# Kernel tuning notes

Measured on AMD Instinct MI355X. Metric: run time of the kernel, lower is better.

Reference implementation:

```python
import jax, jax.numpy as jnp
import numpy as np

B, T = 8, 2048
IN, OUT = 1024, 1024
M, C = 32, 32
MIN_P, MAX_P = 1.0, 1024.0
EPS = 1e-5


def setup_inputs() -> dict:
    key = jax.random.key(0)
    ks = jax.random.split(key, 4)
    x = jax.random.normal(ks[0], (B, T, IN), dtype=jnp.float32)
    # pre: Linear(IN, 2*M + 2*OUT); mix: Linear(2*M*C, OUT)
    pre_w = jax.random.normal(ks[1], (IN, 2 * M + 2 * OUT), dtype=jnp.float32) / np.sqrt(IN)
    pre_b = jnp.zeros((2 * M + 2 * OUT,), jnp.float32)
    mix_w = jax.random.normal(ks[2], (2 * M * C, OUT), dtype=jnp.float32) / np.sqrt(2 * M * C)
    mix_b = jnp.zeros((OUT,), jnp.float32)
    # FFA decay/oscillation params (paper init): gamma_{m,c} = exp(-|a_m| + i b_c)
    a = jnp.linspace(1e-6, 0.5, M, dtype=jnp.float32)
    b = 2.0 * jnp.pi / jnp.linspace(MIN_P, MAX_P, C, dtype=jnp.float32)
    return dict(x=x, pre_w=pre_w, pre_b=pre_b, mix_w=mix_w, mix_b=mix_b, a=a, b=b)


def _ffa(u, a, b):
    """Complex-decay linear recurrence: s_t = gamma * s_{t-1} + u_t (s_0 = 0).

    u: [B,T,M] real input (broadcast over context dim C).
    Returns all states: [B,T,M,C] complex64.
    """
    log_gamma = (-jnp.abs(a))[:, None] + 1j * b[None, :]  # [M,C]
    gamma = jnp.exp(log_gamma).astype(jnp.complex64)
    Tn = u.shape[1]
    h = jnp.broadcast_to(u[..., None].astype(jnp.complex64), u.shape + (C,))  # [B,T,M,C]
    h = jnp.moveaxis(h, 1, 0)  # [T,B,M,C]
    p = jnp.broadcast_to(gamma, (Tn, 1, M, C))  # [T,1,M,C] time-invariant decay

    def combine(e1, e2):
        p1, h1 = e1
        p2, h2 = e2
        return (p1 * p2, h1 * p2 + h2)

    _, hs = jax.lax.associative_scan(combine, (p, h), axis=0)
    return jnp.moveaxis(hs, 0, 1)  # [B,T,M,C]


def reference(x, pre_w, pre_b, mix_w, mix_b, a, b):
    Bx, Tx, _ = x.shape
    pre = x @ pre_w + pre_b  # [B,T,2M+2OUT]
    y, thru, gate = jnp.split(pre, [M, M + OUT], axis=-1)
    gate = jax.nn.sigmoid(gate)
    in_gate, out_gate = gate[..., :M], gate[..., M:]
    s = _ffa(y * in_gate, a, b)  # [B,T,M,C] complex64
    # torch.view_as_real -> [...,M,C,2] then flatten -> interleaved (re,im)
    zr = jnp.stack([s.real, s.imag], axis=-1).reshape(Bx, Tx, 2 * M * C)
    z = zr @ mix_w + mix_b  # [B,T,OUT]
    # LayerNorm (no affine)
    z = (z - z.mean(-1, keepdims=True)) / jnp.sqrt(z.var(-1, keepdims=True) + EPS)
    out = z * out_gate + thru * (1.0 - out_gate)
    return out, s
```

## Files before the change

### kernel.cpp

```cpp
#include <hip/hip_runtime.h>
#include <stdint.h>

typedef __attribute__((ext_vector_type(2))) __bf16 bf16x2;
typedef __attribute__((ext_vector_type(4))) __bf16 bf16x4;
typedef __attribute__((ext_vector_type(8))) __bf16 bf16x8;
typedef __attribute__((ext_vector_type(4))) float f32x4;

#define DEV __device__ __forceinline__

DEV void g2lds16(const void* g, void* l) {
  __builtin_amdgcn_global_load_lds(
      (const __attribute__((address_space(1))) void*)g,
      (__attribute__((address_space(3))) void*)l, 16, 0, 0);
}

__global__ __launch_bounds__(256) void cvt_f32_bf16(const float* __restrict__ s,
                                                    __bf16* __restrict__ d, int n) {
  int i = (blockIdx.x * 256 + threadIdx.x) * 4;
  if (i >= n) return;
  float4 v = *reinterpret_cast<const float4*>(s + i);
  bf16x4 o;
  o[0] = (__bf16)v.x; o[1] = (__bf16)v.y; o[2] = (__bf16)v.z; o[3] = (__bf16)v.w;
  *reinterpret_cast<bf16x4*>(d + i) = o;
}

__global__ __launch_bounds__(256) void transpose_to_bf16(const float* __restrict__ src,
                                                         __bf16* __restrict__ dst,
                                                         int K, int N, int Npad) {
  __shared__ float tile[32][33];
  int n0 = blockIdx.x * 32, k0 = blockIdx.y * 32;
  int tx = threadIdx.x & 31, ty = threadIdx.x >> 5;
#pragma unroll
  for (int j = 0; j < 4; ++j) {
    int k = k0 + ty + j * 8;
    int n = n0 + tx;
    float v = 0.f;
    if (n < N) v = src[(long)k * N + n];
    tile[ty + j * 8][tx] = v;
  }
  __syncthreads();
#pragma unroll
  for (int j = 0; j < 4; ++j) {
    int n = n0 + ty + j * 8;
    int k = k0 + tx;
    if (n < Npad) dst[(long)n * K + k] = (__bf16)tile[tx][ty + j * 8];
  }
}

template <bool OUT_BF16>
__global__ __launch_bounds__(256) void gemm_mfma(const __bf16* __restrict__ A,
                                                 const __bf16* __restrict__ Wt,
                                                 const float* __restrict__ bias,
                                                 void* __restrict__ Cout,
                                                 int K, int Nreal, int ldc) {
  __shared__ __bf16 As[2][128 * 32];
  __shared__ __bf16 Bs[2][128 * 32];
  const int tid = threadIdx.x;
  const int lane = tid & 63, wid = tid >> 6;

  const int nwg = gridDim.x * gridDim.y;
  const int orig = blockIdx.y * gridDim.x + blockIdx.x;
  const int wg = ((orig & 7) * (nwg >> 3)) + (orig >> 3);
  const int tm = (wg / gridDim.x) * 128, tn = (wg % gridDim.x) * 128;

  const int wr = (wid >> 1) * 64, wc = (wid & 1) * 64;

  f32x4 acc[4][4] = {};

  const int r0 = tid >> 2, c0 = (tid & 3) * 8;
  const int r1 = r0 + 64;

  int aoff[4], boff[4];
#pragma unroll
  for (int i = 0; i < 4; ++i) {
    aoff[i] = (wr + i * 16 + (lane & 15)) * 32 + (lane >> 4) * 8;
    boff[i] = (wc + i * 16 + (lane & 15)) * 32 + (lane >> 4) * 8;
  }

  const __bf16* Arow0 = A + (long)(tm + r0) * K + c0;
  const __bf16* Arow1 = A + (long)(tm + r1) * K + c0;
  const __bf16* Wrow0 = Wt + (long)(tn + r0) * K + c0;
  const __bf16* Wrow1 = Wt + (long)(tn + r1) * K + c0;

  g2lds16(Arow0, As[0] + tid * 8);
  g2lds16(Arow1, As[0] + (tid + 256) * 8);
  g2lds16(Wrow0, Bs[0] + tid * 8);
  g2lds16(Wrow1, Bs[0] + (tid + 256) * 8);
  __syncthreads();

  const int nt = K >> 5;
  int cur = 0;
  for (int t = 1; t < nt; ++t) {
    const int k0 = t << 5;
    const int nxt = cur ^ 1;
    g2lds16(Arow0 + k0, As[nxt] + tid * 8);
    g2lds16(Arow1 + k0, As[nxt] + (tid + 256) * 8);
    g2lds16(Wrow0 + k0, Bs[nxt] + tid * 8);
    g2lds16(Wrow1 + k0, Bs[nxt] + (tid + 256) * 8);
    bf16x8 af[4], bw[4];
#pragma unroll
    for (int i = 0; i < 4; ++i) af[i] = *reinterpret_cast<const bf16x8*>(&As[cur][aoff[i]]);
#pragma unroll
    for (int i = 0; i < 4; ++i) bw[i] = *reinterpret_cast<const bf16x8*>(&Bs[cur][boff[i]]);
#pragma unroll
    for (int mi = 0; mi < 4; ++mi)
#pragma unroll
      for (int ni = 0; ni < 4; ++ni)
        acc[mi][ni] = __builtin_amdgcn_mfma_f32_16x16x32_bf16(af[mi], bw[ni],
                                                              acc[mi][ni], 0, 0, 0);
    __syncthreads();
    cur = nxt;
  }
  {
    bf16x8 af[4], bw[4];
#pragma unroll
    for (int i = 0; i < 4; ++i) af[i] = *reinterpret_cast<const bf16x8*>(&As[cur][aoff[i]]);
#pragma unroll
    for (int i = 0; i < 4; ++i) bw[i] = *reinterpret_cast<const bf16x8*>(&Bs[cur][boff[i]]);
#pragma unroll
    for (int mi = 0; mi < 4; ++mi)
#pragma unroll
      for (int ni = 0; ni < 4; ++ni)
        acc[mi][ni] = __builtin_amdgcn_mfma_f32_16x16x32_bf16(af[mi], bw[ni],
                                                              acc[mi][ni], 0, 0, 0);
  }

  const int rbase = tm + wr + ((lane >> 4) * 4);
  const int cbase = tn + wc + (lane & 15);
#pragma unroll
  for (int mi = 0; mi < 4; ++mi) {
#pragma unroll
    for (int ni = 0; ni < 4; ++ni) {
      int col = cbase + ni * 16;
      if (col < Nreal) {
        float bv = bias[col];
#pragma unroll
        for (int r = 0; r < 4; ++r) {
          long row = rbase + mi * 16 + r;
          float v = acc[mi][ni][r] + bv;
          if (OUT_BF16) ((__bf16*)Cout)[row * ldc + col] = (__bf16)v;
          else          ((float*)Cout)[row * ldc + col] = v;
        }
      }
    }
  }
}

__global__ __launch_bounds__(256) void u_kernel(const __bf16* __restrict__ pre,
                                                float* __restrict__ u) {
  int i = blockIdx.x * 8 + (threadIdx.x >> 5);
  int m = threadIdx.x & 31;
  const __bf16* pr = pre + (long)i * 2112;
  float y = (float)pr[m];
  float g = (float)pr[1056 + m];
  float sg = 1.f / (1.f + expf(-g));
  int b = i >> 11, t = i & 2047;
  u[(long)((b * 32) + m) * 2048 + t] = y * sg;
}

__global__ __launch_bounds__(64) void scan_kernel(const float* __restrict__ u,
                                                  const float* __restrict__ a,
                                                  const float* __restrict__ bfr,
                                                  __bf16* __restrict__ s_bf,
                                                  float* __restrict__ s_re) {
  int blk = blockIdx.x;
  int b = blk >> 4, mp = blk & 15;
  int lane = threadIdx.x;
  int mh = lane >> 5, c = lane & 31;
  int m = mp * 2 + mh;
  const float* ub = u + (long)(b * 32 + m) * 2048;
  float decay = expf(-fabsf(a[m]));
  float gr = decay * cosf(bfr[c]);
  float gi = decay * sinf(bfr[c]);
  float sr = 0.f, si = 0.f;
  long base = (long)b * 2048 * 1024 + m * 32 + c;
  for (int t = 0; t < 2048; ++t) {
    float uv = ub[t];
    float nr = fmaf(gr, sr, fmaf(-gi, si, uv));
    float ni_ = fmaf(gr, si, gi * sr);
    sr = nr; si = ni_;
    long ci = base + (long)t * 1024;
    bf16x2 zv; zv[0] = (__bf16)sr; zv[1] = (__bf16)si;
    *reinterpret_cast<bf16x2*>(s_bf + 2 * ci) = zv;
    s_re[ci] = sr;
  }
}

__global__ __launch_bounds__(256) void ln_gate_kernel(float* __restrict__ z,
                                                      const __bf16* __restrict__ pre) {
  __shared__ float rs[4], rss[4];
  long row = blockIdx.x;
  float* zp = z + row * 1024;
  int tid = threadIdx.x;
  float4 v = *reinterpret_cast<const float4*>(zp + tid * 4);
  float s = v.x + v.y + v.z + v.w;
  float ss = v.x * v.x + v.y * v.y + v.z * v.z + v.w * v.w;
#pragma unroll
  for (int o = 32; o > 0; o >>= 1) {
    s += __shfl_down(s, o, 64);
    ss += __shfl_down(ss, o, 64);
  }
  if ((tid & 63) == 0) { rs[tid >> 6] = s; rss[tid >> 6] = ss; }
  __syncthreads();
  s = rs[0] + rs[1] + rs[2] + rs[3];
  ss = rss[0] + rss[1] + rss[2] + rss[3];
  float mean = s * (1.f / 1024.f);
  float var = ss * (1.f / 1024.f) - mean * mean;
  float rstd = rsqrtf(var + 1e-5f);
  const __bf16* pr = pre + row * 2112;
  bf16x4 th = *reinterpret_cast<const bf16x4*>(pr + 32 + tid * 4);
  bf16x4 og = *reinterpret_cast<const bf16x4*>(pr + 1088 + tid * 4);
  float4 o; float g;
  g = 1.f / (1.f + expf(-(float)og[0])); o.x = (v.x - mean) * rstd * g + (float)th[0] * (1.f - g);
  g = 1.f / (1.f + expf(-(float)og[1])); o.y = (v.y - mean) * rstd * g + (float)th[1] * (1.f - g);
  g = 1.f / (1.f + expf(-(float)og[2])); o.z = (v.z - mean) * rstd * g + (float)th[2] * (1.f - g);
  g = 1.f / (1.f + expf(-(float)og[3])); o.w = (v.w - mean) * rstd * g + (float)th[3] * (1.f - g);
  *reinterpret_cast<float4*>(zp + tid * 4) = o;
}

extern "C" void kernel_launch(void* const* d_in, const int* in_sizes, int n_in,
                              void* d_out, int out_size, void* d_ws, size_t ws_size,
                              hipStream_t stream) {
  const float* x = (const float*)d_in[0];
  const float* pre_w = (const float*)d_in[1];
  const float* pre_b = (const float*)d_in[2];
  const float* mix_w = (const float*)d_in[3];
  const float* mix_b = (const float*)d_in[4];
  const float* a = (const float*)d_in[5];
  const float* bfr = (const float*)d_in[6];

  char* ws = (char*)d_ws;
  __bf16* buf0  = (__bf16*)(ws + 0);
  __bf16* preWT = (__bf16*)(ws + 67108864);
  __bf16* mixWT = (__bf16*)(ws + 71565312);
  __bf16* pre   = (__bf16*)(ws + 75759616);
  float*  u     = (float*)(ws + 144965632);
  const size_t WS_NEEDED = 147062784ull;
  if (ws_size < WS_NEEDED) return;

  __bf16* x_bf = buf0;
  __bf16* s_bf = buf0;

  float* out0 = (float*)d_out;
  float* s_re = out0 + 16777216;

  cvt_f32_bf16<<<16384, 256, 0, stream>>>(x, x_bf, 16777216);
  transpose_to_bf16<<<dim3(68, 32), 256, 0, stream>>>(pre_w, preWT, 1024, 2112, 2176);
  transpose_to_bf16<<<dim3(32, 64), 256, 0, stream>>>(mix_w, mixWT, 2048, 1024, 1024);
  gemm_mfma<true><<<dim3(17, 128), 256, 0, stream>>>(x_bf, preWT, pre_b, pre,
                                                     1024, 2112, 2112);
  u_kernel<<<2048, 256, 0, stream>>>(pre, u);
  scan_kernel<<<128, 64, 0, stream>>>(u, a, bfr, s_bf, s_re);
  gemm_mfma<false><<<dim3(8, 128), 256, 0, stream>>>(s_bf, mixWT, mix_b, out0,
                                                     2048, 1024, 1024);
  ln_gate_kernel<<<16384, 256, 0, stream>>>(out0, pre);
}
```

Before: 361.3 us.

## Replace GEMM with 256x256-tile 8-wave kernel using phased LDS pipelining

Replaces the 128x128-tile, 4-wave bf16 MFMA GEMM with a 256x256-tile, 512-thread kernel. Each block stages 64-wide K chunks into double-buffered LDS with a swizzled layout, and splits the compute into four phases whose loads are interleaved with MFMAs using explicit barriers, waitcnts and setprio. The aim is more data reuse per LDS byte, fewer bank conflicts, and overlap of global-to-LDS copies with compute. The two weight transposes now share one workspace buffer, with the mix_w transpose moved after the first GEMM. Costs are higher register and LDS pressure and padding of the pre GEMM's N dimension to 2304, which wastes some work.

```diff
diff --git a/kernel.cpp b/kernel.cpp
--- a/kernel.cpp
+++ b/kernel.cpp
@@ -12,6 +12,14 @@
   __builtin_amdgcn_global_load_lds(
       (const __attribute__((address_space(1))) void*)g,
       (__attribute__((address_space(3))) void*)l, 16, 0, 0);
+}
+
+DEV void barrier_ws() {
+  __builtin_amdgcn_sched_barrier(0);
+  asm volatile("" ::: "memory");
+  __builtin_amdgcn_s_barrier();
+  asm volatile("" ::: "memory");
+  __builtin_amdgcn_sched_barrier(0);
 }
 
 __global__ __launch_bounds__(256) void cvt_f32_bf16(const float* __restrict__ s,
@@ -47,99 +55,121 @@
   }
 }
 
+#define STAGE_A(d, kh, kc)                                           \
+  { g2lds16(A + aoffg0 + (kc), &As[d][(kh)*8192 + q0 * 8]);          \
+    g2lds16(A + aoffg1 + (kc), &As[d][(kh)*8192 + q1 * 8]); }
+#define STAGE_B(d, kh, kc)                                           \
+  { g2lds16(Wt + boffg0 + (kc), &Bs[d][(kh)*8192 + q0 * 8]);         \
+    g2lds16(Wt + boffg1 + (kc), &Bs[d][(kh)*8192 + q1 * 8]); }
+
+#define PHASE(d, MQ, KH, READB, STAGE_STMT, TAILWAIT)                         \
+  {                                                                           \
+    bf16x8 af[4];                                                             \
+    _Pragma("unroll") for (int i = 0; i < 4; ++i)                             \
+        af[i] = *reinterpret_cast<const bf16x8*>(                             \
+            &As[d][(KH)*8192 + aoffl[(MQ)*4 + i]]);                           \
+    if (READB) {                                                              \
+      _Pragma("unroll") for (int n = 0; n < 4; ++n)                           \
+          bw[n] = *reinterpret_cast<const bf16x8*>(                           \
+              &Bs[d][(KH)*8192 + boffl[n]]);                                  \
+    }                                                                         \
+    STAGE_STMT;                                                               \
+    barrier_ws();                                                             \
+    __builtin_amdgcn_s_setprio(1);                                            \
+    _Pragma("unroll") for (int i = 0; i < 4; ++i)                             \
+      _Pragma("unroll") for (int n = 0; n < 4; ++n)                           \
+          acc[(MQ)*4 + i][n] = __builtin_amdgcn_mfma_f32_16x16x32_bf16(       \
+              af[i], bw[n], acc[(MQ)*4 + i][n], 0, 0, 0);                     \
+    __builtin_amdgcn_s_setprio(0);                                            \
+    TAILWAIT;                                                                 \
+    barrier_ws();                                                             \
+  }
+
 template <bool OUT_BF16>
-__global__ __launch_bounds__(256) void gemm_mfma(const __bf16* __restrict__ A,
-                                                 const __bf16* __restrict__ Wt,
-                                                 const float* __restrict__ bias,
-                                                 void* __restrict__ Cout,
-                                                 int K, int Nreal, int ldc) {
-  __shared__ __bf16 As[2][128 * 32];
-  __shared__ __bf16 Bs[2][128 * 32];
+__global__ __launch_bounds__(512, 2) void gemm_8p(const __bf16* __restrict__ A,
+                                                  const __bf16* __restrict__ Wt,
+                                                  const float* __restrict__ bias,
+                                                  void* __restrict__ Cout,
+                                                  int K, int Nreal, int ldc,
+                                                  int gx) {
+  __shared__ __bf16 As[2][16384];
+  __shared__ __bf16 Bs[2][16384];
   const int tid = threadIdx.x;
   const int lane = tid & 63, wid = tid >> 6;
-
-  const int nwg = gridDim.x * gridDim.y;
-  const int orig = blockIdx.y * gridDim.x + blockIdx.x;
+  const int wr = wid >> 2, wc = wid & 3;
+
+  const int nwg = gridDim.x;
+  const int orig = blockIdx.x;
   const int wg = ((orig & 7) * (nwg >> 3)) + (orig >> 3);
-  const int tm = (wg / gridDim.x) * 128, tn = (wg % gridDim.x) * 128;
-
-  const int wr = (wid >> 1) * 64, wc = (wid & 1) * 64;
-
-  f32x4 acc[4][4] = {};
-
-  const int r0 = tid >> 2, c0 = (tid & 3) * 8;
-  const int r1 = r0 + 64;
-
-  int aoff[4], boff[4];
-#pragma unroll
-  for (int i = 0; i < 4; ++i) {
-    aoff[i] = (wr + i * 16 + (lane & 15)) * 32 + (lane >> 4) * 8;
-    boff[i] = (wc + i * 16 + (lane & 15)) * 32 + (lane >> 4) * 8;
-  }
-
-  const __bf16* Arow0 = A + (long)(tm + r0) * K + c0;
-  const __bf16* Arow1 = A + (long)(tm + r1) * K + c0;
-  const __bf16* Wrow0 = Wt + (long)(tn + r0) * K + c0;
-  const __bf16* Wrow1 = Wt + (long)(tn + r1) * K + c0;
-
-  g2lds16(Arow0, As[0] + tid * 8);
-  g2lds16(Arow1, As[0] + (tid + 256) * 8);
-  g2lds16(Wrow0, Bs[0] + tid * 8);
-  g2lds16(Wrow1, Bs[0] + (tid + 256) * 8);
-  __syncthreads();
-
-  const int nt = K >> 5;
-  int cur = 0;
-  for (int t = 1; t < nt; ++t) {
-    const int k0 = t << 5;
-    const int nxt = cur ^ 1;
-    g2lds16(Arow0 + k0, As[nxt] + tid * 8);
-    g2lds16(Arow1 + k0, As[nxt] + (tid + 256) * 8);
-    g2lds16(Wrow0 + k0, Bs[nxt] + tid * 8);
-    g2lds16(Wrow1 + k0, Bs[nxt] + (tid + 256) * 8);
-    bf16x8 af[4], bw[4];
-#pragma unroll
-    for (int i = 0; i < 4; ++i) af[i] = *reinterpret_cast<const bf16x8*>(&As[cur][aoff[i]]);
-#pragma unroll
-    for (int i = 0; i < 4; ++i) bw[i] = *reinterpret_cast<const bf16x8*>(&Bs[cur][boff[i]]);
-#pragma unroll
-    for (int mi = 0; mi < 4; ++mi)
-#pragma unroll
-      for (int ni = 0; ni < 4; ++ni)
-        acc[mi][ni] = __builtin_amdgcn_mfma_f32_16x16x32_bf16(af[mi], bw[ni],
-                                                              acc[mi][ni], 0, 0, 0);
-    __syncthreads();
-    cur = nxt;
+  const int tm = (wg / gx) * 256, tn = (wg % gx) * 256;
+
+  f32x4 acc[8][4] = {};
+  bf16x8 bw[4];
+
+  const int q0 = tid, q1 = tid + 512;
+  const int row0 = ((q0 >> 3) << 1) | ((q0 >> 2) & 1);
+  const int c0e = (((q0 & 3) - (q0 >> 3)) & 3) * 8;
+  const int row1 = ((q1 >> 3) << 1) | ((q1 >> 2) & 1);
+  const int c1e = (((q1 & 3) - (q1 >> 3)) & 3) * 8;
+  const long aoffg0 = (long)(tm + row0) * K + c0e;
+  const long aoffg1 = (long)(tm + row1) * K + c1e;
+  const long boffg0 = (long)(tn + row0) * K + c0e;
+  const long boffg1 = (long)(tn + row1) * K + c1e;
+
+  const int l15 = lane & 15, cl = lane >> 4;
+  int aoffl[8], boffl[4];
+#pragma unroll
+  for (int mf = 0; mf < 8; ++mf) {
+    int row = wr * 128 + (mf >> 2) * 64 + (mf & 3) * 16 + l15;
+    aoffl[mf] = (row >> 1) * 64 + (((row & 1) << 2) | ((cl + (row >> 1)) & 3)) * 8;
+  }
+#pragma unroll
+  for (int nf = 0; nf < 4; ++nf) {
+    int row = wc * 64 + nf * 16 + l15;
+    boffl[nf] = (row >> 1) * 64 + (((row & 1) << 2) | ((cl + (row >> 1)) & 3)) * 8;
+  }
+
+  STAGE_A(0, 0, 0);
+  STAGE_B(0, 0, 0);
+  STAGE_A(0, 1, 32);
+  STAGE_B(0, 1, 32);
+  asm volatile("s_waitcnt vmcnt(4)" ::: "memory");
+  barrier_ws();
+
+  const int nt = K >> 6;
+  for (int T = 0; T < nt - 1; ++T) {
+    const int d = T & 1, e = d ^ 1;
+    const int kc = (T + 1) << 6;
+    PHASE(d, 0, 0, 1, STAGE_A(e, 0, kc), ((void)0));
+    PHASE(d, 1, 0, 0, STAGE_B(e, 0, kc),
+          asm volatile("s_waitcnt vmcnt(4)" ::: "memory"));
+    PHASE(d, 0, 1, 1, STAGE_A(e, 1, kc + 32), ((void)0));
+    PHASE(d, 1, 1, 0, STAGE_B(e, 1, kc + 32),
+          asm volatile("s_waitcnt vmcnt(4)" ::: "memory"));
   }
   {
-    bf16x8 af[4], bw[4];
-#pragma unroll
-    for (int i = 0; i < 4; ++i) af[i] = *reinterpret_cast<const bf16x8*>(&As[cur][aoff[i]]);
-#pragma unroll
-    for (int i = 0; i < 4; ++i) bw[i] = *reinterpret_cast<const bf16x8*>(&Bs[cur][boff[i]]);
-#pragma unroll
-    for (int mi = 0; mi < 4; ++mi)
-#pragma unroll
-      for (int ni = 0; ni < 4; ++ni)
-        acc[mi][ni] = __builtin_amdgcn_mfma_f32_16x16x32_bf16(af[mi], bw[ni],
-                                                              acc[mi][ni], 0, 0, 0);
-  }
-
-  const int rbase = tm + wr + ((lane >> 4) * 4);
-  const int cbase = tn + wc + (lane & 15);
-#pragma unroll
-  for (int mi = 0; mi < 4; ++mi) {
-#pragma unroll
-    for (int ni = 0; ni < 4; ++ni) {
-      int col = cbase + ni * 16;
+    const int d = (nt - 1) & 1;
+    PHASE(d, 0, 0, 1, ((void)0), ((void)0));
+    PHASE(d, 1, 0, 0, ((void)0),
+          asm volatile("s_waitcnt vmcnt(0)" ::: "memory"));
+    PHASE(d, 0, 1, 1, ((void)0), ((void)0));
+    PHASE(d, 1, 1, 0, ((void)0), ((void)0));
+  }
+
+#pragma unroll
+  for (int mf = 0; mf < 8; ++mf) {
+    const int rg = tm + wr * 128 + (mf >> 2) * 64 + (mf & 3) * 16 + (lane >> 4) * 4;
+#pragma unroll
+    for (int nf = 0; nf < 4; ++nf) {
+      int col = tn + wc * 64 + nf * 16 + l15;
       if (col < Nreal) {
         float bv = bias[col];
 #pragma unroll
         for (int r = 0; r < 4; ++r) {
-          long row = rbase + mi * 16 + r;
-          float v = acc[mi][ni][r] + bv;
-          if (OUT_BF16) ((__bf16*)Cout)[row * ldc + col] = (__bf16)v;
-          else          ((float*)Cout)[row * ldc + col] = v;
+          long row = rg + r;
+          float v = acc[mf][nf][r] + bv;
+          if (OUT_BF16) ((__bf16*)Cout)[row * (long)ldc + col] = (__bf16)v;
+          else          ((float*)Cout)[row * (long)ldc + col] = v;
         }
       }
     }
@@ -231,11 +261,10 @@
 
   char* ws = (char*)d_ws;
   __bf16* buf0  = (__bf16*)(ws + 0);
-  __bf16* preWT = (__bf16*)(ws + 67108864);
-  __bf16* mixWT = (__bf16*)(ws + 71565312);
-  __bf16* pre   = (__bf16*)(ws + 75759616);
-  float*  u     = (float*)(ws + 144965632);
-  const size_t WS_NEEDED = 147062784ull;
+  __bf16* wtbuf = (__bf16*)(ws + 67108864);
+  __bf16* pre   = (__bf16*)(ws + 71827456);
+  float*  u     = (float*)(ws + 141033472);
+  const size_t WS_NEEDED = 143130624ull;
   if (ws_size < WS_NEEDED) return;
 
   __bf16* x_bf = buf0;
@@ -245,13 +274,11 @@
   float* s_re = out0 + 16777216;
 
   cvt_f32_bf16<<<16384, 256, 0, stream>>>(x, x_bf, 16777216);
-  transpose_to_bf16<<<dim3(68, 32), 256, 0, stream>>>(pre_w, preWT, 1024, 2112, 2176);
-  transpose_to_bf16<<<dim3(32, 64), 256, 0, stream>>>(mix_w, mixWT, 2048, 1024, 1024);
-  gemm_mfma<true><<<dim3(17, 128), 256, 0, stream>>>(x_bf, preWT, pre_b, pre,
-                                                     1024, 2112, 2112);
+  transpose_to_bf16<<<dim3(72, 32), 256, 0, stream>>>(pre_w, wtbuf, 1024, 2112, 2304);
+  gemm_8p<true><<<576, 512, 0, stream>>>(x_bf, wtbuf, pre_b, pre, 1024, 2112, 2112, 9);
   u_kernel<<<2048, 256, 0, stream>>>(pre, u);
+  transpose_to_bf16<<<dim3(32, 64), 256, 0, stream>>>(mix_w, wtbuf, 2048, 1024, 1024);
   scan_kernel<<<128, 64, 0, stream>>>(u, a, bfr, s_bf, s_re);
-  gemm_mfma<false><<<dim3(8, 128), 256, 0, stream>>>(s_bf, mixWT, mix_b, out0,
-                                                     2048, 1024, 1024);
+  gemm_8p<false><<<256, 512, 0, stream>>>(s_bf, wtbuf, mix_b, out0, 2048, 1024, 1024, 4);
   ln_gate_kernel<<<16384, 256, 0, stream>>>(out0, pre);
 }
```

New measurement: 339.9 us. -5.9%, faster.
